# Kernel optimization log

Measured on AMD Instinct MI355X. Metric: run time of the kernel, lower is better.

Reference implementation:

```python
import jax, jax.numpy as jnp
import numpy as np

B, N, E, P, PH, H = 4, 512, 768, 64, 32, 8
D = E // H  # 96
FFN = 3072

def _ln(x, g, b, eps=1e-5):
    mu = jnp.mean(x, axis=-1, keepdims=True)
    var = jnp.mean((x - mu) ** 2, axis=-1, keepdims=True)
    return (x - mu) * jax.lax.rsqrt(var + eps) * g + b

def setup_inputs() -> dict:
    key = jax.random.key(0)
    ks = iter(jax.random.split(key, 80))
    def f(*s):
        return jax.random.normal(next(ks), s, jnp.float32) * 0.02
    ones = lambda *s: jnp.ones(s, jnp.float32)
    zeros = lambda *s: jnp.zeros(s, jnp.float32)
    return {
        'x': jax.random.normal(next(ks), (B, N, E), jnp.float32),
        'pair': jax.random.normal(next(ks), (B, N, N, P), jnp.float32) * 0.5,
        'attn_mask': zeros(B, 1, N, N),
        'op_mask': ones(B, N, 1),
        'op_norm': ones(1) / N,
        'nlist': jax.random.randint(next(ks), (B, N, 64), 0, N),
        'wq': f(E, E), 'wk': f(E, E), 'wv': f(E, E),
        'wg': f(E, E), 'bg': zeros(E),
        'wo': f(E, E), 'bo': zeros(E),
        'ln_pair_g': ones(P), 'ln_pair_b': zeros(P),
        'wb': f(H, P), 'bb': zeros(H),
        'ln_attn_g': ones(E), 'ln_attn_b': zeros(E),
        'ln_ffn_g': ones(E), 'ln_ffn_b': zeros(E),
        'w_ffn1': f(FFN, E), 'b_ffn1': zeros(FFN),
        'w_ffn2': f(E, FFN), 'b_ffn2': zeros(E),
        'ln_opm_g': ones(E), 'ln_opm_b': zeros(E),
        'w_opm_in': f(2 * PH, E), 'b_opm_in': zeros(2 * PH),
        'w_opm_out': f(P, PH * PH), 'b_opm_out': zeros(P),
        'ln_tm_g': ones(P), 'ln_tm_b': zeros(P),
        'w_tm_abp': f(2 * PH, P), 'b_tm_abp': zeros(2 * PH),
        'w_tm_abg': f(2 * PH, P), 'b_tm_abg': zeros(2 * PH),
        'w_tm_g': f(P, P), 'b_tm_g': zeros(P),
        'w_tm_z': f(P, PH), 'b_tm_z': zeros(P),
        'ln_tmo_g': ones(PH), 'ln_tmo_b': zeros(PH),
        'ln_pffn_g': ones(P), 'ln_pffn_b': zeros(P),
        'w_pffn1': f(P, P), 'b_pffn1': zeros(P),
        'w_pffn2': f(P, P), 'b_pffn2': zeros(P),
    }

def _forward(x, pair, attn_mask, op_mask, op_norm, wq, wk, wv, wg, bg, wo, bo,
             ln_pair_g, ln_pair_b, wb, bb, ln_attn_g, ln_attn_b,
             ln_ffn_g, ln_ffn_b, w_ffn1, b_ffn1, w_ffn2, b_ffn2,
             ln_opm_g, ln_opm_b, w_opm_in, b_opm_in, w_opm_out, b_opm_out,
             ln_tm_g, ln_tm_b, w_tm_abp, b_tm_abp, w_tm_abg, b_tm_abg,
             w_tm_g, b_tm_g, w_tm_z, b_tm_z, ln_tmo_g, ln_tmo_b,
             ln_pffn_g, ln_pffn_b, w_pffn1, b_pffn1, w_pffn2, b_pffn2):
    Bx, Nx, _ = x.shape
    # --- gated pair-bias self-attention (pre-LN, eval mode: dropout = identity) ---
    h = _ln(x, ln_attn_g, ln_attn_b)
    pn = _ln(pair, ln_pair_g, ln_pair_b)               # AtomAttention pair LayerNorm
    bias = jnp.einsum('bijp,hp->bhij', pn, wb) + bb[None, :, None, None]
    q = (h @ wq.T).reshape(Bx, Nx, H, D).transpose(0, 2, 1, 3) * (D ** -0.5)
    k = (h @ wk.T).reshape(Bx, Nx, H, D).transpose(0, 2, 1, 3)
    v = (h @ wv.T).reshape(Bx, Nx, H, D).transpose(0, 2, 1, 3)
    attn = jax.nn.softmax(jnp.einsum('bhid,bhjd->bhij', q, k) + attn_mask + bias, axis=-1)
    o = jnp.einsum('bhij,bhjd->bhid', attn, v).transpose(0, 2, 1, 3).reshape(Bx, Nx, E)
    o = jax.nn.sigmoid(h @ wg.T + bg) * o              # sigmoid output gate
    x = x + (o @ wo.T + bo)
    # --- atom transition MLP ---
    h = _ln(x, ln_ffn_g, ln_ffn_b)
    x = x + (jax.nn.gelu(h @ w_ffn1.T + b_ffn1, approximate=False) @ w_ffn2.T + b_ffn2)
    # --- OuterProduct pair update (fused: avoids [B,N,N,PH*PH] intermediate) ---
    h = _ln(x, ln_opm_g, ln_opm_b)
    ab = (h @ w_opm_in.T + b_opm_in) * op_mask
    a_o, b_o = jnp.split(ab, 2, axis=-1)               # each [B,N,PH]
    z = jnp.einsum('bid,bje,pde->bijp', a_o, b_o, w_opm_out.reshape(P, PH, PH)) + b_opm_out
    pair = pair + z * op_norm
    # --- triangle multiplication ---
    zp = _ln(pair, ln_tm_g, ln_tm_b)
    gpr = zp @ w_tm_g.T + b_tm_g                       # gate (no sigmoid, matches source)
    ab = (zp @ w_tm_abp.T + b_tm_abp) * jax.nn.sigmoid(zp @ w_tm_abg.T + b_tm_abg)
    a_t, b_t = jnp.split(ab, 2, axis=-1)               # each [B,N,N,PH]
    t = jnp.einsum('bijh,bkjh->bhik', a_t, b_t) + jnp.einsum('bjih,bjkh->bhik', a_t, b_t)
    t = _ln(t.transpose(0, 2, 3, 1), ln_tmo_g, ln_tmo_b) @ w_tm_z.T + b_tm_z
    pair = pair + gpr * t
    # --- pair transition MLP ---
    zp = _ln(pair, ln_pffn_g, ln_pffn_b)
    pair = pair + (jax.nn.gelu(zp @ w_pffn1.T + b_pffn1, approximate=False) @ w_pffn2.T + b_pffn2)
    return x, pair

def reference(x, pair, attn_mask, op_mask, op_norm, nlist, wq, wk, wv, wg, bg, wo, bo,
              ln_pair_g, ln_pair_b, wb, bb, ln_attn_g, ln_attn_b,
              ln_ffn_g, ln_ffn_b, w_ffn1, b_ffn1, w_ffn2, b_ffn2,
              ln_opm_g, ln_opm_b, w_opm_in, b_opm_in, w_opm_out, b_opm_out,
              ln_tm_g, ln_tm_b, w_tm_abp, b_tm_abp, w_tm_abg, b_tm_abg,
              w_tm_g, b_tm_g, w_tm_z, b_tm_z, ln_tmo_g, ln_tmo_b,
              ln_pffn_g, ln_pffn_b, w_pffn1, b_pffn1, w_pffn2, b_pffn2):
    del nlist  # accepted by the torch module but unused in the math
    return _forward(x, pair, attn_mask, op_mask, op_norm, wq, wk, wv, wg, bg, wo, bo,
                    ln_pair_g, ln_pair_b, wb, bb, ln_attn_g, ln_attn_b,
                    ln_ffn_g, ln_ffn_b, w_ffn1, b_ffn1, w_ffn2, b_ffn2,
                    ln_opm_g, ln_opm_b, w_opm_in, b_opm_in, w_opm_out, b_opm_out,
                    ln_tm_g, ln_tm_b, w_tm_abp, b_tm_abp, w_tm_abg, b_tm_abg,
                    w_tm_g, b_tm_g, w_tm_z, b_tm_z, ln_tmo_g, ln_tmo_b,
                    ln_pffn_g, ln_pffn_b, w_pffn1, b_pffn1, w_pffn2, b_pffn2)
```

## Files before the change

kernel.cpp:

```cpp
#include <hip/hip_runtime.h>
#include <hip/hip_bf16.h>
#include <math.h>

#define Nn 512
#define Ee 768
#define Pp 64
#define PHh 32
#define Hh 8
#define Dd 96
#define NNe 262144
#define LNEPS 1e-5f

typedef __attribute__((ext_vector_type(8))) short bf8;
typedef __attribute__((ext_vector_type(4))) short bf4;
typedef __attribute__((ext_vector_type(4))) float f32x4;
#define MFMA(a,b,c) __builtin_amdgcn_mfma_f32_16x16x32_bf16(a,b,c,0,0,0)

__device__ __forceinline__ short f2bf(float f) {
  unsigned u = __builtin_bit_cast(unsigned, f);
  unsigned r = (u + 0x7fffu + ((u >> 16) & 1u)) >> 16;
  return (short)r;
}
__device__ __forceinline__ float bf2f(short s) {
  unsigned u = ((unsigned)(unsigned short)s) << 16;
  return __builtin_bit_cast(float, u);
}

__device__ __forceinline__ float wave_red_sum(float v) {
#pragma unroll
  for (int off = 32; off > 0; off >>= 1) v += __shfl_xor(v, off);
  return v;
}
__device__ __forceinline__ float gelu_exact(float v) {
  return 0.5f * v * (1.f + erff(v * 0.70710678118654752f));
}
__device__ __forceinline__ float sigmoidf_(float v) {
  return 1.f / (1.f + expf(-v));
}

__global__ __launch_bounds__(256) void castw_kernel(
    const float* __restrict__ wq, const float* __restrict__ wk,
    const float* __restrict__ wv, const float* __restrict__ wg,
    const float* __restrict__ wo, const float* __restrict__ f1,
    const float* __restrict__ f2, const float* __restrict__ wop,
    short* __restrict__ dst, float qs) {
  long i = (long)blockIdx.x * 256 + threadIdx.x;
  float v;
  if (i < 589824) v = wq[i] * qs;
  else if (i < 1179648) v = wk[i - 589824];
  else if (i < 1769472) v = wv[i - 1179648];
  else if (i < 2359296) v = wg[i - 1769472];
  else if (i < 2949120) v = wo[i - 2359296];
  else if (i < 5308416) v = f1[i - 2949120];
  else if (i < 7667712) v = f2[i - 5308416];
  else if (i < 7716864) v = wop[i - 7667712];
  else return;
  dst[i] = f2bf(v);
}

__global__ __launch_bounds__(256) void castw2_kernel(
    const float* __restrict__ wb, const float* __restrict__ abp,
    const float* __restrict__ abg, const float* __restrict__ wtg,
    const float* __restrict__ wtz, const float* __restrict__ p1,
    const float* __restrict__ p2, short* __restrict__ dst) {
  int i = blockIdx.x * 256 + threadIdx.x;
  float v;
  if (i < 512) v = wb[i];
  else if (i < 4608) v = abp[i - 512];
  else if (i < 8704) v = abg[i - 4608];
  else if (i < 12800) v = wtg[i - 8704];
  else if (i < 14848) v = wtz[i - 12800];
  else if (i < 18944) v = p1[i - 14848];
  else if (i < 23040) v = p2[i - 18944];
  else return;
  dst[i] = f2bf(v);
}

__global__ __launch_bounds__(256) void ln_bf_kernel(const float* __restrict__ in,
                                                    short* __restrict__ out,
                                                    const float* __restrict__ gam,
                                                    const float* __restrict__ bet, int C) {
  int row = blockIdx.x;
  const float* xr = in + (long)row * C;
  short* yr = out + (long)row * C;
  float s = 0.f, ss = 0.f;
  for (int c = threadIdx.x; c < C; c += 256) { float v = xr[c]; s += v; ss += v * v; }
  s = wave_red_sum(s); ss = wave_red_sum(ss);
  __shared__ float sm[4][2];
  int wv = threadIdx.x >> 6, lane = threadIdx.x & 63;
  if (lane == 0) { sm[wv][0] = s; sm[wv][1] = ss; }
  __syncthreads();
  float ts = sm[0][0] + sm[1][0] + sm[2][0] + sm[3][0];
  float tss = sm[0][1] + sm[1][1] + sm[2][1] + sm[3][1];
  float mu = ts / C;
  float var = tss / C - mu * mu;
  float rs = rsqrtf(var + LNEPS);
  for (int c = threadIdx.x; c < C; c += 256) {
    float v = xr[c];
    yr[c] = f2bf((v - mu) * rs * gam[c] + bet[c]);
  }
}

__global__ __launch_bounds__(256) void gemm_bf(
    const short* __restrict__ A, int lda, long asB, long asH,
    const short* __restrict__ Bm, int ldb, long bsB, long bsH,
    float* __restrict__ outF, int ldf, long fsB, long fsH,
    short* __restrict__ outB, int ldob,
    const float* __restrict__ resid, int ldr, long rsB, long rsH,
    const float* __restrict__ bias,
    int M, int N, int K, int act, int vtrans, int Hdim) {
  int bz = blockIdx.z, bb = bz / Hdim, hh = bz % Hdim;
  A += bb * asB + hh * asH;
  Bm += bb * bsB + hh * bsH;
  if (outF) outF += bb * fsB + hh * fsH;
  if (outB) outB += bb * fsB + hh * fsH;
  if (resid) resid += bb * rsB + hh * rsH;
  __shared__ __align__(16) short As[64 * 40];
  __shared__ __align__(16) short Bs[64 * 40];
  int m0 = blockIdx.y * 64, n0 = blockIdx.x * 64;
  int tid = threadIdx.x;
  int wv = tid >> 6, lane = tid & 63;
  int wr = wv >> 1, wc = wv & 1;
  int lhi = lane >> 4, llo = lane & 15;
  int r4 = tid >> 2, c8 = (tid & 3) * 8;
  f32x4 acc[2][2] = {};
  for (int k0 = 0; k0 < K; k0 += 32) {
    *(bf8*)&As[r4 * 40 + c8] = *(const bf8*)(A + (long)(m0 + r4) * lda + k0 + c8);
    bf8 bv = {};
    if (n0 + r4 < N) bv = *(const bf8*)(Bm + (long)(n0 + r4) * ldb + k0 + c8);
    *(bf8*)&Bs[r4 * 40 + c8] = bv;
    __syncthreads();
    bf8 a0 = *(const bf8*)&As[(wr * 32 + llo) * 40 + lhi * 8];
    bf8 a1 = *(const bf8*)&As[(wr * 32 + 16 + llo) * 40 + lhi * 8];
    bf8 b0 = *(const bf8*)&Bs[(wc * 32 + llo) * 40 + lhi * 8];
    bf8 b1 = *(const bf8*)&Bs[(wc * 32 + 16 + llo) * 40 + lhi * 8];
    acc[0][0] = MFMA(a0, b0, acc[0][0]);
    acc[0][1] = MFMA(a0, b1, acc[0][1]);
    acc[1][0] = MFMA(a1, b0, acc[1][0]);
    acc[1][1] = MFMA(a1, b1, acc[1][1]);
    __syncthreads();
  }
#pragma unroll
  for (int mi = 0; mi < 2; ++mi) {
    int gmb = m0 + wr * 32 + mi * 16 + lhi * 4;
#pragma unroll
    for (int ni = 0; ni < 2; ++ni) {
      int gn = n0 + wc * 32 + ni * 16 + llo;
      if (gn >= N) continue;
      float bv = bias ? bias[gn] : 0.f;
      float vr[4];
#pragma unroll
      for (int r = 0; r < 4; ++r) {
        float v = acc[mi][ni][r] + bv;
        if (resid) {
          float rv = resid[(long)(gmb + r) * ldr + gn];
          if (act == 2) v = sigmoidf_(rv) * acc[mi][ni][r];
          else v += rv;
        }
        if (act == 1) v = gelu_exact(v);
        vr[r] = v;
      }
      if (outF) {
#pragma unroll
        for (int r = 0; r < 4; ++r) outF[(long)(gmb + r) * ldf + gn] = vr[r];
      }
      if (outB) {
        if (vtrans) {
          bf4 pk;
#pragma unroll
          for (int r = 0; r < 4; ++r) pk[r] = f2bf(vr[r]);
          *(bf4*)(outB + ((long)((gmb >> 9) * 768 + gn) * 512 + (gmb & 511))) = pk;
        } else {
#pragma unroll
          for (int r = 0; r < 4; ++r) outB[(long)(gmb + r) * ldob + gn] = f2bf(vr[r]);
        }
      }
    }
  }
}

__global__ __launch_bounds__(256) void gemm_qkvg(
    const short* __restrict__ A, const short* __restrict__ W,
    short* __restrict__ q_bf, short* __restrict__ k_bf,
    short* __restrict__ vT_bf, float* __restrict__ gb,
    const float* __restrict__ bg) {
  __shared__ __align__(16) short As[64 * 40];
  __shared__ __align__(16) short Bs[64 * 40];
  int m0 = blockIdx.y * 64, n0 = blockIdx.x * 64;
  int sec = n0 / 768;
  int cbase = n0 - sec * 768;
  int tid = threadIdx.x;
  int wv = tid >> 6, lane = tid & 63;
  int wr = wv >> 1, wc = wv & 1;
  int lhi = lane >> 4, llo = lane & 15;
  int r4 = tid >> 2, c8 = (tid & 3) * 8;
  f32x4 acc[2][2] = {};
  for (int k0 = 0; k0 < 768; k0 += 32) {
    *(bf8*)&As[r4 * 40 + c8] = *(const bf8*)(A + (long)(m0 + r4) * 768 + k0 + c8);
    *(bf8*)&Bs[r4 * 40 + c8] = *(const bf8*)(W + (long)(n0 + r4) * 768 + k0 + c8);
    __syncthreads();
    bf8 a0 = *(const bf8*)&As[(wr * 32 + llo) * 40 + lhi * 8];
    bf8 a1 = *(const bf8*)&As[(wr * 32 + 16 + llo) * 40 + lhi * 8];
    bf8 b0 = *(const bf8*)&Bs[(wc * 32 + llo) * 40 + lhi * 8];
    bf8 b1 = *(const bf8*)&Bs[(wc * 32 + 16 + llo) * 40 + lhi * 8];
    acc[0][0] = MFMA(a0, b0, acc[0][0]);
    acc[0][1] = MFMA(a0, b1, acc[0][1]);
    acc[1][0] = MFMA(a1, b0, acc[1][0]);
    acc[1][1] = MFMA(a1, b1, acc[1][1]);
    __syncthreads();
  }
#pragma unroll
  for (int mi = 0; mi < 2; ++mi) {
    int gmb = m0 + wr * 32 + mi * 16 + lhi * 4;
#pragma unroll
    for (int ni = 0; ni < 2; ++ni) {
      int cn = cbase + wc * 32 + ni * 16 + llo;
      if (sec == 0) {
#pragma unroll
        for (int r = 0; r < 4; ++r) q_bf[(long)(gmb + r) * 768 + cn] = f2bf(acc[mi][ni][r]);
      } else if (sec == 1) {
#pragma unroll
        for (int r = 0; r < 4; ++r) k_bf[(long)(gmb + r) * 768 + cn] = f2bf(acc[mi][ni][r]);
      } else if (sec == 2) {
        bf4 pk;
#pragma unroll
        for (int r = 0; r < 4; ++r) pk[r] = f2bf(acc[mi][ni][r]);
        *(bf4*)(vT_bf + ((long)((gmb >> 9) * 768 + cn) * 512 + (gmb & 511))) = pk;
      } else {
        float bv = bg[cn];
#pragma unroll
        for (int r = 0; r < 4; ++r) gb[(long)(gmb + r) * 768 + cn] = acc[mi][ni][r] + bv;
      }
    }
  }
}

__global__ __launch_bounds__(256) void attn_fused(
    const short* __restrict__ q_bf, const short* __restrict__ k_bf,
    const short* __restrict__ bias_bf, const float* __restrict__ mask,
    short* __restrict__ out_bf) {
  int it = blockIdx.x, h = blockIdx.y, b = blockIdx.z;
  int tid = threadIdx.x;
  int wv = tid >> 6, lane = tid & 63;
  int lhi = lane >> 4, llo = lane & 15;
  int i0 = it * 16;
  long qoff = ((long)(b * 512 + i0)) * 768 + h * 96;
  bf8 qf[3];
#pragma unroll
  for (int ks = 0; ks < 3; ++ks)
    qf[ks] = *(const bf8*)(q_bf + qoff + (long)llo * 768 + ks * 32 + lhi * 8);
  long koff = ((long)b * 512) * 768 + h * 96;
  long bioff = (long)(b * 8 + h) * NNe + (long)i0 * 512;
  long moff = (long)b * NNe + (long)i0 * 512;
  float sv[8][4];
  int jb0 = wv * 128;
#pragma unroll
  for (int jf = 0; jf < 8; ++jf) {
    int jb = jb0 + jf * 16;
    f32x4 acc = {0.f, 0.f, 0.f, 0.f};
#pragma unroll
    for (int ks = 0; ks < 3; ++ks) {
      bf8 kf = *(const bf8*)(k_bf + koff + (long)(jb + llo) * 768 + ks * 32 + lhi * 8);
      acc = MFMA(qf[ks], kf, acc);
    }
#pragma unroll
    for (int r = 0; r < 4; ++r) {
      int irow = lhi * 4 + r;
      int j = jb + llo;
      float bia = bf2f(bias_bf[bioff + (long)irow * 512 + j]);
      float mk = mask[moff + (long)irow * 512 + j];
      sv[jf][r] = acc[r] + bia + mk;
    }
  }
  __shared__ float redA[4][20];
  __shared__ float redB[4][20];
  float rmax[4];
#pragma unroll
  for (int r = 0; r < 4; ++r) {
    float m = sv[0][r];
#pragma unroll
    for (int jf = 1; jf < 8; ++jf) m = fmaxf(m, sv[jf][r]);
#pragma unroll
    for (int off = 1; off < 16; off <<= 1) m = fmaxf(m, __shfl_xor(m, off, 16));
    if (llo == 0) redA[wv][lhi * 4 + r] = m;
  }
  __syncthreads();
#pragma unroll
  for (int r = 0; r < 4; ++r) {
    int row = lhi * 4 + r;
    rmax[r] = fmaxf(fmaxf(redA[0][row], redA[1][row]),
                    fmaxf(redA[2][row], redA[3][row]));
  }
  float rsum[4] = {0.f, 0.f, 0.f, 0.f};
#pragma unroll
  for (int jf = 0; jf < 8; ++jf)
#pragma unroll
    for (int r = 0; r < 4; ++r) {
      float e = __expf(sv[jf][r] - rmax[r]);
      sv[jf][r] = e;
      rsum[r] += e;
    }
#pragma unroll
  for (int r = 0; r < 4; ++r) {
#pragma unroll
    for (int off = 1; off < 16; off <<= 1) rsum[r] += __shfl_xor(rsum[r], off, 16);
    if (llo == 0) redB[wv][lhi * 4 + r] = rsum[r];
  }
  __syncthreads();
#pragma unroll
  for (int r = 0; r < 4; ++r) {
    int row = lhi * 4 + r;
    float s = redB[0][row] + redB[1][row] + redB[2][row] + redB[3][row];
    float inv = 1.f / s;
#pragma unroll
    for (int jf = 0; jf < 8; ++jf) {
      int j = jb0 + jf * 16 + llo;
      out_bf[bioff + (long)row * 512 + j] = f2bf(sv[jf][r] * inv);
    }
  }
}

__global__ __launch_bounds__(256) void opmask_kernel(float* __restrict__ ab,
                                                     const float* __restrict__ mask,
                                                     short* __restrict__ bo_bf) {
  int idx = blockIdx.x * 256 + threadIdx.x;
  if (idx < 131072) {
    float v = ab[idx] * mask[idx >> 6];
    ab[idx] = v;
    int ch = idx & 63;
    if (ch >= 32) bo_bf[(idx >> 6) * 32 + ch - 32] = f2bf(v);
  }
}

__global__ __launch_bounds__(256) void opm_T_kernel(const float* __restrict__ ab,
                                                    const float* __restrict__ w,
                                                    short* __restrict__ T) {
  int p = blockIdx.y;
  int row = blockIdx.x * 8 + threadIdx.y;
  int e = threadIdx.x;
  const float* a = ab + (long)row * 64;
  const float* wp = w + p * 1024 + e;
  float acc = 0.f;
#pragma unroll
  for (int d = 0; d < 32; ++d) acc += a[d] * wp[d * 32];
  T[((long)row * 64 + p) * 32 + e] = f2bf(acc);
}

__global__ __launch_bounds__(256) void pair_bias_mfma(
    const float* __restrict__ pair, const float* __restrict__ gam,
    const float* __restrict__ bet, const short* __restrict__ wb_a,
    const float* __restrict__ bbv, short* __restrict__ bias) {
  __shared__ __align__(16) short Zb[64 * 72];
  __shared__ __align__(16) short Wb[16 * 72];
  __shared__ float sp[4][2][72];
  int tid = threadIdx.x;
  long e0 = (long)blockIdx.x * 64;
  int b = (int)(e0 >> 18);
  long ein = e0 & (NNe - 1);
  const float* base = pair + e0 * 64;
  for (int l = tid; l < 1024; l += 256) {
    int h = l >> 6, c = l & 63;
    Wb[h * 72 + c] = (h < 8) ? wb_a[h * 64 + c] : (short)0;
  }
  int e = tid & 63, q = tid >> 6;
  f32x4 v4[4];
  float s = 0.f, ss = 0.f;
#pragma unroll
  for (int k = 0; k < 4; ++k) {
    v4[k] = *(const f32x4*)(base + (long)e * 64 + q * 16 + k * 4);
#pragma unroll
    for (int u = 0; u < 4; ++u) { float v = v4[k][u]; s += v; ss += v * v; }
  }
  sp[q][0][e] = s; sp[q][1][e] = ss;
  __syncthreads();
  float ts = sp[0][0][e] + sp[1][0][e] + sp[2][0][e] + sp[3][0][e];
  float tss = sp[0][1][e] + sp[1][1][e] + sp[2][1][e] + sp[3][1][e];
  float mu = ts * 0.015625f, var = tss * 0.015625f - mu * mu;
  float rs = rsqrtf(var + LNEPS);
#pragma unroll
  for (int k = 0; k < 4; ++k) {
    bf4 pk;
#pragma unroll
    for (int u = 0; u < 4; ++u) {
      int c = q * 16 + k * 4 + u;
      pk[u] = f2bf((v4[k][u] - mu) * rs * gam[c] + bet[c]);
    }
    *(bf4*)&Zb[e * 72 + q * 16 + k * 4] = pk;
  }
  __syncthreads();
  int wv = tid >> 6, lane = tid & 63;
  int lhi = lane >> 4, llo = lane & 15;
  int n0 = wv * 16;
  f32x4 acc = {0.f, 0.f, 0.f, 0.f};
#pragma unroll
  for (int ks = 0; ks < 2; ++ks) {
    bf8 a = *(const bf8*)&Wb[llo * 72 + ks * 32 + lhi * 8];
    bf8 bz = *(const bf8*)&Zb[(n0 + llo) * 72 + ks * 32 + lhi * 8];
    acc = MFMA(a, bz, acc);
  }
  int elem = n0 + llo;
#pragma unroll
  for (int r = 0; r < 4; ++r) {
    int h = lhi * 4 + r;
    if (h < 8) bias[(long)(b * 8 + h) * NNe + ein + elem] = f2bf(acc[r] + bbv[h]);
  }
}

__global__ __launch_bounds__(256) void opm_ab_fused(
    const float* __restrict__ pair_in, const short* __restrict__ Tb,
    const short* __restrict__ bo_bf, const float* __restrict__ b_out,
    const float* __restrict__ op_norm, const float* __restrict__ gam,
    const float* __restrict__ bet, const short* __restrict__ wp_a,
    const float* __restrict__ b_abp, const short* __restrict__ wg_a,
    const float* __restrict__ b_abg, float* __restrict__ pair1,
    short* __restrict__ aN, short* __restrict__ bN) {
  int jt = blockIdx.x;
  int i = blockIdx.y;
  int tid = threadIdx.x;
  __shared__ __align__(16) short Tsb[64 * 40];
  __shared__ __align__(16) short Bob[64 * 40];
  __shared__ __align__(16) short Zb[64 * 72];
  __shared__ __align__(16) short Wp[64 * 72];
  __shared__ __align__(16) short Wg[64 * 72];
  __shared__ float spS[64][9];
  __shared__ float spQ[64][9];
  int wv = tid >> 6, lane = tid & 63;
  int wr = wv >> 1, wc = wv & 1;
  int lhi = lane >> 4, llo = lane & 15;
  int chb = wr * 32 + lhi * 4;
  {
    int p = tid >> 2, e8 = (tid & 3) * 8;
    *(bf8*)&Tsb[p * 40 + e8] = *(const bf8*)(Tb + (long)i * 2048 + p * 32 + e8);
    *(bf8*)&Bob[p * 40 + e8] = *(const bf8*)(bo_bf + (long)(jt * 64 + p) * 32 + e8);
  }
  for (int l = tid; l < 512; l += 256) {
    int r = l >> 3, c8 = (l & 7) * 8;
    *(bf8*)&Wp[r * 72 + c8] = *(const bf8*)(wp_a + r * 64 + c8);
    *(bf8*)&Wg[r * 72 + c8] = *(const bf8*)(wg_a + r * 64 + c8);
  }
  long ebase = (long)i * 512 + jt * 64;
  const float* pbase = pair_in + ebase * 64;
  f32x4 x[2][2];
#pragma unroll
  for (int mi = 0; mi < 2; ++mi)
#pragma unroll
    for (int ni = 0; ni < 2; ++ni)
      x[mi][ni] = *(const f32x4*)(pbase + (long)(wc * 32 + ni * 16 + llo) * 64 +
                                  chb + mi * 16);
  __syncthreads();
  f32x4 acc[2][2] = {};
  {
    bf8 a0 = *(const bf8*)&Tsb[(wr * 32 + llo) * 40 + lhi * 8];
    bf8 a1 = *(const bf8*)&Tsb[(wr * 32 + 16 + llo) * 40 + lhi * 8];
    bf8 b0 = *(const bf8*)&Bob[(wc * 32 + llo) * 40 + lhi * 8];
    bf8 b1 = *(const bf8*)&Bob[(wc * 32 + 16 + llo) * 40 + lhi * 8];
    acc[0][0] = MFMA(a0, b0, acc[0][0]);
    acc[0][1] = MFMA(a0, b1, acc[0][1]);
    acc[1][0] = MFMA(a1, b0, acc[1][0]);
    acc[1][1] = MFMA(a1, b1, acc[1][1]);
  }
  float nrm = op_norm[0];
#pragma unroll
  for (int mi = 0; mi < 2; ++mi) {
    f32x4 bo4 = *(const f32x4*)(b_out + chb + mi * 16);
#pragma unroll
    for (int ni = 0; ni < 2; ++ni)
#pragma unroll
      for (int r = 0; r < 4; ++r)
        x[mi][ni][r] += (acc[mi][ni][r] + bo4[r]) * nrm;
  }
#pragma unroll
  for (int mi = 0; mi < 2; ++mi)
#pragma unroll
    for (int ni = 0; ni < 2; ++ni)
      *(f32x4*)(pair1 + (ebase + wc * 32 + ni * 16 + llo) * 64 + chb + mi * 16) =
          x[mi][ni];
#pragma unroll
  for (int ni = 0; ni < 2; ++ni) {
    float s = 0.f, ss = 0.f;
#pragma unroll
    for (int mi = 0; mi < 2; ++mi)
#pragma unroll
      for (int r = 0; r < 4; ++r) { float v = x[mi][ni][r]; s += v; ss += v * v; }
    int e = wc * 32 + ni * 16 + llo;
    spS[e][wr * 4 + lhi] = s;
    spQ[e][wr * 4 + lhi] = ss;
  }
  __syncthreads();
  float mu1[2], rs1[2];
#pragma unroll
  for (int ni = 0; ni < 2; ++ni) {
    int e = wc * 32 + ni * 16 + llo;
    float s = 0.f, q2 = 0.f;
#pragma unroll
    for (int k = 0; k < 8; ++k) { s += spS[e][k]; q2 += spQ[e][k]; }
    float mu = s * 0.015625f, var = q2 * 0.015625f - mu * mu;
    mu1[ni] = mu; rs1[ni] = rsqrtf(var + LNEPS);
  }
#pragma unroll
  for (int mi = 0; mi < 2; ++mi) {
    f32x4 gv = *(const f32x4*)(gam + chb + mi * 16);
    f32x4 bv = *(const f32x4*)(bet + chb + mi * 16);
#pragma unroll
    for (int ni = 0; ni < 2; ++ni) {
      int e = wc * 32 + ni * 16 + llo;
      bf4 pk;
#pragma unroll
      for (int r = 0; r < 4; ++r)
        pk[r] = f2bf((x[mi][ni][r] - mu1[ni]) * rs1[ni] * gv[r] + bv[r]);
      *(bf4*)&Zb[e * 72 + chb + mi * 16] = pk;
    }
  }
  __syncthreads();
  f32x4 ap[2][2] = {};
  f32x4 ag[2][2] = {};
#pragma unroll
  for (int ks = 0; ks < 2; ++ks) {
    bf8 z0 = *(const bf8*)&Zb[(wr * 32 + llo) * 72 + ks * 32 + lhi * 8];
    bf8 z1 = *(const bf8*)&Zb[(wr * 32 + 16 + llo) * 72 + ks * 32 + lhi * 8];
    bf8 p0 = *(const bf8*)&Wp[(wc * 32 + llo) * 72 + ks * 32 + lhi * 8];
    bf8 p1 = *(const bf8*)&Wp[(wc * 32 + 16 + llo) * 72 + ks * 32 + lhi * 8];
    bf8 g0 = *(const bf8*)&Wg[(wc * 32 + llo) * 72 + ks * 32 + lhi * 8];
    bf8 g1 = *(const bf8*)&Wg[(wc * 32 + 16 + llo) * 72 + ks * 32 + lhi * 8];
    ap[0][0] = MFMA(z0, p0, ap[0][0]);
    ap[0][1] = MFMA(z0, p1, ap[0][1]);
    ap[1][0] = MFMA(z1, p0, ap[1][0]);
    ap[1][1] = MFMA(z1, p1, ap[1][1]);
    ag[0][0] = MFMA(z0, g0, ag[0][0]);
    ag[0][1] = MFMA(z0, g1, ag[0][1]);
    ag[1][0] = MFMA(z1, g0, ag[1][0]);
    ag[1][1] = MFMA(z1, g1, ag[1][1]);
  }
#pragma unroll
  for (int mi = 0; mi < 2; ++mi) {
    int elemb = wr * 32 + mi * 16 + lhi * 4;
#pragma unroll
    for (int ni = 0; ni < 2; ++ni) {
      int ch = wc * 32 + ni * 16 + llo;
      float bp = b_abp[ch], bg = b_abg[ch];
      bf4 pack;
#pragma unroll
      for (int r = 0; r < 4; ++r)
        pack[r] = f2bf((ap[mi][ni][r] + bp) * sigmoidf_(ag[mi][ni][r] + bg));
      short* dst = (ch < 32) ? (aN + (long)ch * NNe) : (bN + (long)(ch - 32) * NNe);
      *(bf4*)(dst + ebase + elemb) = pack;
    }
  }
}

__global__ __launch_bounds__(256) void tm_tri_mfma(const short* __restrict__ aN,
                                                   const short* __restrict__ bN,
                                                   short* __restrict__ t_out) {
  int h = blockIdx.z;
  int i0 = blockIdx.y * 64, k0 = blockIdx.x * 64;
  const short* A = aN + (long)h * NNe;
  const short* B = bN + (long)h * NNe;
  __shared__ __align__(16) short A1[64 * 40];
  __shared__ __align__(16) short B1[64 * 40];
  __shared__ __align__(16) short A2[64 * 40];
  __shared__ __align__(16) short B2[64 * 40];
  int tid = threadIdx.x;
  int wv = tid >> 6, lane = tid & 63;
  int wr = wv >> 1, wc = wv & 1;
  int lhi = lane >> 4, llo = lane & 15;
  int r1 = tid >> 2, cp = (tid & 3) * 8;
  int s2 = tid >> 4;
  int cg = (tid & 15) * 4;
  f32x4 acc[2][2] = {};
  for (int j0 = 0; j0 < 512; j0 += 32) {
    *(bf8*)&A1[r1 * 40 + cp] = *(const bf8*)(A + (long)(i0 + r1) * 512 + j0 + cp);
    *(bf8*)&B1[r1 * 40 + cp] = *(const bf8*)(B + (long)(k0 + r1) * 512 + j0 + cp);
    bf4 va0 = *(const bf4*)(A + (long)(j0 + 2 * s2) * 512 + i0 + cg);
    bf4 va1 = *(const bf4*)(A + (long)(j0 + 2 * s2 + 1) * 512 + i0 + cg);
    bf4 vb0 = *(const bf4*)(B + (long)(j0 + 2 * s2) * 512 + k0 + cg);
    bf4 vb1 = *(const bf4*)(B + (long)(j0 + 2 * s2 + 1) * 512 + k0 + cg);
#pragma unroll
    for (int q = 0; q < 4; ++q) {
      unsigned pa = (unsigned)(unsigned short)va0[q] |
                    ((unsigned)(unsigned short)va1[q] << 16);
      unsigned pb = (unsigned)(unsigned short)vb0[q] |
                    ((unsigned)(unsigned short)vb1[q] << 16);
      *(unsigned*)&A2[(cg + q) * 40 + 2 * s2] = pa;
      *(unsigned*)&B2[(cg + q) * 40 + 2 * s2] = pb;
    }
    __syncthreads();
    bf8 a0 = *(const bf8*)&A1[(wr * 32 + llo) * 40 + lhi * 8];
    bf8 a1 = *(const bf8*)&A1[(wr * 32 + 16 + llo) * 40 + lhi * 8];
    bf8 b0 = *(const bf8*)&B1[(wc * 32 + llo) * 40 + lhi * 8];
    bf8 b1 = *(const bf8*)&B1[(wc * 32 + 16 + llo) * 40 + lhi * 8];
    acc[0][0] = MFMA(a0, b0, acc[0][0]);
    acc[0][1] = MFMA(a0, b1, acc[0][1]);
    acc[1][0] = MFMA(a1, b0, acc[1][0]);
    acc[1][1] = MFMA(a1, b1, acc[1][1]);
    bf8 c0 = *(const bf8*)&A2[(wr * 32 + llo) * 40 + lhi * 8];
    bf8 c1 = *(const bf8*)&A2[(wr * 32 + 16 + llo) * 40 + lhi * 8];
    bf8 d0 = *(const bf8*)&B2[(wc * 32 + llo) * 40 + lhi * 8];
    bf8 d1 = *(const bf8*)&B2[(wc * 32 + 16 + llo) * 40 + lhi * 8];
    acc[0][0] = MFMA(c0, d0, acc[0][0]);
    acc[0][1] = MFMA(c0, d1, acc[0][1]);
    acc[1][0] = MFMA(c1, d0, acc[1][0]);
    acc[1][1] = MFMA(c1, d1, acc[1][1]);
    __syncthreads();
  }
  short* tp = t_out + (long)h * NNe;
#pragma unroll
  for (int mi = 0; mi < 2; ++mi)
#pragma unroll
    for (int ni = 0; ni < 2; ++ni) {
      int row = i0 + wr * 32 + mi * 16 + lhi * 4;
      int col = k0 + wc * 32 + ni * 16 + llo;
#pragma unroll
      for (int r = 0; r < 4; ++r) tp[(long)(row + r) * 512 + col] = f2bf(acc[mi][ni][r]);
    }
}

__global__ __launch_bounds__(256) void upd_pffn_fused(
    float* __restrict__ pb, const short* __restrict__ t_in,
    const float* __restrict__ g_tm, const float* __restrict__ b_tm,
    const short* __restrict__ wg_a, const float* __restrict__ b_g,
    const short* __restrict__ wz_a, const float* __restrict__ b_z,
    const float* __restrict__ g_tmo, const float* __restrict__ b_tmo,
    const float* __restrict__ g_pf, const float* __restrict__ b_pf,
    const short* __restrict__ w1_a, const float* __restrict__ b1,
    const short* __restrict__ w2_a, const float* __restrict__ b2) {
  __shared__ __align__(16) short Zb[64 * 72];
  __shared__ __align__(16) short Tlb[64 * 40];
  __shared__ __align__(16) short Wbuf[64 * 72];
  __shared__ __align__(16) short Wzb[64 * 40];
  __shared__ float spS[64][9];
  __shared__ float spQ[64][9];
  __shared__ float spB[4][2][72];
  int tid = threadIdx.x;
  long e0 = (long)blockIdx.x * 64;
  float* base = pb + e0 * 64;
  int wv = tid >> 6, lane = tid & 63;
  int wr = wv >> 1, wc = wv & 1;
  int lhi = lane >> 4, llo = lane & 15;
  int chb = wr * 32 + lhi * 4;
  int r0 = tid >> 3, c0 = (tid & 7) * 8;
  int r1 = (tid + 256) >> 3, c1 = ((tid + 256) & 7) * 8;
  bf8 w1r0, w1r1, w2r0, w2r1;
  {
    *(bf8*)&Wbuf[r0 * 72 + c0] = *(const bf8*)(wg_a + r0 * 64 + c0);
    *(bf8*)&Wbuf[r1 * 72 + c1] = *(const bf8*)(wg_a + r1 * 64 + c1);
    w1r0 = *(const bf8*)(w1_a + r0 * 64 + c0);
    w1r1 = *(const bf8*)(w1_a + r1 * 64 + c1);
    w2r0 = *(const bf8*)(w2_a + r0 * 64 + c0);
    w2r1 = *(const bf8*)(w2_a + r1 * 64 + c1);
    int rz = tid >> 2, cz = (tid & 3) * 8;
    *(bf8*)&Wzb[rz * 40 + cz] = *(const bf8*)(wz_a + rz * 32 + cz);
  }
  f32x4 x[2][2];
#pragma unroll
  for (int mi = 0; mi < 2; ++mi)
#pragma unroll
    for (int ni = 0; ni < 2; ++ni)
      x[mi][ni] = *(const f32x4*)(base + (long)(wc * 32 + ni * 16 + llo) * 64 +
                                  chb + mi * 16);
#pragma unroll
  for (int ni = 0; ni < 2; ++ni) {
    float s = 0.f, ss = 0.f;
#pragma unroll
    for (int mi = 0; mi < 2; ++mi)
#pragma unroll
      for (int r = 0; r < 4; ++r) { float v = x[mi][ni][r]; s += v; ss += v * v; }
    int e = wc * 32 + ni * 16 + llo;
    spS[e][wr * 4 + lhi] = s;
    spQ[e][wr * 4 + lhi] = ss;
  }
  int te = tid & 63, tq = tid >> 6;
  float tt[8];
  {
    float sB = 0.f, ssB = 0.f;
#pragma unroll
    for (int k = 0; k < 8; ++k) {
      float v = bf2f(t_in[(long)(tq * 8 + k) * NNe + e0 + te]);
      tt[k] = v; sB += v; ssB += v * v;
    }
    spB[tq][0][te] = sB; spB[tq][1][te] = ssB;
  }
  __syncthreads();
  {
    float ts = spB[0][0][te] + spB[1][0][te] + spB[2][0][te] + spB[3][0][te];
    float tss = spB[0][1][te] + spB[1][1][te] + spB[2][1][te] + spB[3][1][te];
    float mu = ts * 0.03125f, var = tss * 0.03125f - mu * mu;
    float rs = rsqrtf(var + LNEPS);
    bf8 pk;
#pragma unroll
    for (int k = 0; k < 8; ++k) {
      int c = tq * 8 + k;
      pk[k] = f2bf((tt[k] - mu) * rs * g_tmo[c] + b_tmo[c]);
    }
    *(bf8*)&Tlb[te * 40 + tq * 8] = pk;
  }
  float mu1[2], rs1[2];
#pragma unroll
  for (int ni = 0; ni < 2; ++ni) {
    int e = wc * 32 + ni * 16 + llo;
    float s = 0.f, q2 = 0.f;
#pragma unroll
    for (int k = 0; k < 8; ++k) { s += spS[e][k]; q2 += spQ[e][k]; }
    float mu = s * 0.015625f, var = q2 * 0.015625f - mu * mu;
    mu1[ni] = mu; rs1[ni] = rsqrtf(var + LNEPS);
  }
#pragma unroll
  for (int mi = 0; mi < 2; ++mi) {
    f32x4 gv = *(const f32x4*)(g_tm + chb + mi * 16);
    f32x4 bv = *(const f32x4*)(b_tm + chb + mi * 16);
#pragma unroll
    for (int ni = 0; ni < 2; ++ni) {
      int e = wc * 32 + ni * 16 + llo;
      bf4 pk;
#pragma unroll
      for (int r = 0; r < 4; ++r)
        pk[r] = f2bf((x[mi][ni][r] - mu1[ni]) * rs1[ni] * gv[r] + bv[r]);
      *(bf4*)&Zb[e * 72 + chb + mi * 16] = pk;
    }
  }
  __syncthreads();
  f32x4 accg[2][2] = {};
  f32x4 accz[2][2] = {};
#pragma unroll
  for (int ks = 0; ks < 2; ++ks) {
    bf8 a0 = *(const bf8*)&Wbuf[(wr * 32 + llo) * 72 + ks * 32 + lhi * 8];
    bf8 a1 = *(const bf8*)&Wbuf[(wr * 32 + 16 + llo) * 72 + ks * 32 + lhi * 8];
    bf8 z0 = *(const bf8*)&Zb[(wc * 32 + llo) * 72 + ks * 32 + lhi * 8];
    bf8 z1 = *(const bf8*)&Zb[(wc * 32 + 16 + llo) * 72 + ks * 32 + lhi * 8];
    accg[0][0] = MFMA(a0, z0, accg[0][0]);
    accg[0][1] = MFMA(a0, z1, accg[0][1]);
    accg[1][0] = MFMA(a1, z0, accg[1][0]);
    accg[1][1] = MFMA(a1, z1, accg[1][1]);
  }
  {
    bf8 a0 = *(const bf8*)&Wzb[(wr * 32 + llo) * 40 + lhi * 8];
    bf8 a1 = *(const bf8*)&Wzb[(wr * 32 + 16 + llo) * 40 + lhi * 8];
    bf8 t0 = *(const bf8*)&Tlb[(wc * 32 + llo) * 40 + lhi * 8];
    bf8 t1 = *(const bf8*)&Tlb[(wc * 32 + 16 + llo) * 40 + lhi * 8];
    accz[0][0] = MFMA(a0, t0, accz[0][0]);
    accz[0][1] = MFMA(a0, t1, accz[0][1]);
    accz[1][0] = MFMA(a1, t0, accz[1][0]);
    accz[1][1] = MFMA(a1, t1, accz[1][1]);
  }
#pragma unroll
  for (int mi = 0; mi < 2; ++mi) {
    f32x4 bgv = *(const f32x4*)(b_g + chb + mi * 16);
    f32x4 bzv = *(const f32x4*)(b_z + chb + mi * 16);
#pragma unroll
    for (int ni = 0; ni < 2; ++ni)
#pragma unroll
      for (int r = 0; r < 4; ++r)
        x[mi][ni][r] += (accg[mi][ni][r] + bgv[r]) * (accz[mi][ni][r] + bzv[r]);
  }
#pragma unroll
  for (int ni = 0; ni < 2; ++ni) {
    float s = 0.f, ss = 0.f;
#pragma unroll
    for (int mi = 0; mi < 2; ++mi)
#pragma unroll
      for (int r = 0; r < 4; ++r) { float v = x[mi][ni][r]; s += v; ss += v * v; }
    int e = wc * 32 + ni * 16 + llo;
    spS[e][wr * 4 + lhi] = s;
    spQ[e][wr * 4 + lhi] = ss;
  }
  __syncthreads();
  *(bf8*)&Wbuf[r0 * 72 + c0] = w1r0;
  *(bf8*)&Wbuf[r1 * 72 + c1] = w1r1;
#pragma unroll
  for (int ni = 0; ni < 2; ++ni) {
    int e = wc * 32 + ni * 16 + llo;
    float s = 0.f, q2 = 0.f;
#pragma unroll
    for (int k = 0; k < 8; ++k) { s += spS[e][k]; q2 += spQ[e][k]; }
    float mu = s * 0.015625f, var = q2 * 0.015625f - mu * mu;
    mu1[ni] = mu; rs1[ni] = rsqrtf(var + LNEPS);
  }
#pragma unroll
  for (int mi = 0; mi < 2; ++mi) {
    f32x4 gv = *(const f32x4*)(g_pf + chb + mi * 16);
    f32x4 bv = *(const f32x4*)(b_pf + chb + mi * 16);
#pragma unroll
    for (int ni = 0; ni < 2; ++ni) {
      int e = wc * 32 + ni * 16 + llo;
      bf4 pk;
#pragma unroll
      for (int r = 0; r < 4; ++r)
        pk[r] = f2bf((x[mi][ni][r] - mu1[ni]) * rs1[ni] * gv[r] + bv[r]);
      *(bf4*)&Zb[e * 72 + chb + mi * 16] = pk;
    }
  }
  __syncthreads();
  f32x4 acc1[2][2] = {};
#pragma unroll
  for (int ks = 0; ks < 2; ++ks) {
    bf8 a0 = *(const bf8*)&Wbuf[(wr * 32 + llo) * 72 + ks * 32 + lhi * 8];
    bf8 a1 = *(const bf8*)&Wbuf[(wr * 32 + 16 + llo) * 72 + ks * 32 + lhi * 8];
    bf8 z0 = *(const bf8*)&Zb[(wc * 32 + llo) * 72 + ks * 32 + lhi * 8];
    bf8 z1 = *(const bf8*)&Zb[(wc * 32 + 16 + llo) * 72 + ks * 32 + lhi * 8];
    acc1[0][0] = MFMA(a0, z0, acc1[0][0]);
    acc1[0][1] = MFMA(a0, z1, acc1[0][1]);
    acc1[1][0] = MFMA(a1, z0, acc1[1][0]);
    acc1[1][1] = MFMA(a1, z1, acc1[1][1]);
  }
  __syncthreads();
  *(bf8*)&Wbuf[r0 * 72 + c0] = w2r0;
  *(bf8*)&Wbuf[r1 * 72 + c1] = w2r1;
#pragma unroll
  for (int mi = 0; mi < 2; ++mi) {
    f32x4 bv = *(const f32x4*)(b1 + chb + mi * 16);
#pragma unroll
    for (int ni = 0; ni < 2; ++ni) {
      int e = wc * 32 + ni * 16 + llo;
      bf4 pk;
#pragma unroll
      for (int r = 0; r < 4; ++r) pk[r] = f2bf(gelu_exact(acc1[mi][ni][r] + bv[r]));
      *(bf4*)&Zb[e * 72 + chb + mi * 16] = pk;
    }
  }
  __syncthreads();
  f32x4 acc2[2][2] = {};
#pragma unroll
  for (int ks = 0; ks < 2; ++ks) {
    bf8 a0 = *(const bf8*)&Wbuf[(wr * 32 + llo) * 72 + ks * 32 + lhi * 8];
    bf8 a1 = *(const bf8*)&Wbuf[(wr * 32 + 16 + llo) * 72 + ks * 32 + lhi * 8];
    bf8 z0 = *(const bf8*)&Zb[(wc * 32 + llo) * 72 + ks * 32 + lhi * 8];
    bf8 z1 = *(const bf8*)&Zb[(wc * 32 + 16 + llo) * 72 + ks * 32 + lhi * 8];
    acc2[0][0] = MFMA(a0, z0, acc2[0][0]);
    acc2[0][1] = MFMA(a0, z1, acc2[0][1]);
    acc2[1][0] = MFMA(a1, z0, acc2[1][0]);
    acc2[1][1] = MFMA(a1, z1, acc2[1][1]);
  }
#pragma unroll
  for (int mi = 0; mi < 2; ++mi) {
    f32x4 bv = *(const f32x4*)(b2 + chb + mi * 16);
#pragma unroll
    for (int ni = 0; ni < 2; ++ni) {
#pragma unroll
      for (int r = 0; r < 4; ++r) x[mi][ni][r] += acc2[mi][ni][r] + bv[r];
      *(f32x4*)(base + (long)(wc * 32 + ni * 16 + llo) * 64 + chb + mi * 16) =
          x[mi][ni];
    }
  }
}

extern "C" void kernel_launch(void* const* d_in, const int* in_sizes, int n_in,
                              void* d_out, int out_size, void* d_ws, size_t ws_size,
                              hipStream_t stream) {
  const float* x = (const float*)d_in[0];
  const float* pair = (const float*)d_in[1];
  const float* attn_mask = (const float*)d_in[2];
  const float* op_mask = (const float*)d_in[3];
  const float* op_norm = (const float*)d_in[4];
  const float* wq = (const float*)d_in[6];
  const float* wk = (const float*)d_in[7];
  const float* wv_ = (const float*)d_in[8];
  const float* wg = (const float*)d_in[9];
  const float* bg = (const float*)d_in[10];
  const float* wo = (const float*)d_in[11];
  const float* bo = (const float*)d_in[12];
  const float* ln_pair_g = (const float*)d_in[13];
  const float* ln_pair_b = (const float*)d_in[14];
  const float* wb = (const float*)d_in[15];
  const float* bb = (const float*)d_in[16];
  const float* ln_attn_g = (const float*)d_in[17];
  const float* ln_attn_b = (const float*)d_in[18];
  const float* ln_ffn_g = (const float*)d_in[19];
  const float* ln_ffn_b = (const float*)d_in[20];
  const float* w_ffn1 = (const float*)d_in[21];
  const float* b_ffn1 = (const float*)d_in[22];
  const float* w_ffn2 = (const float*)d_in[23];
  const float* b_ffn2 = (const float*)d_in[24];
  const float* ln_opm_g = (const float*)d_in[25];
  const float* ln_opm_b = (const float*)d_in[26];
  const float* w_opm_in = (const float*)d_in[27];
  const float* b_opm_in = (const float*)d_in[28];
  const float* w_opm_out = (const float*)d_in[29];
  const float* b_opm_out = (const float*)d_in[30];
  const float* ln_tm_g = (const float*)d_in[31];
  const float* ln_tm_b = (const float*)d_in[32];
  const float* w_tm_abp = (const float*)d_in[33];
  const float* b_tm_abp = (const float*)d_in[34];
  const float* w_tm_abg = (const float*)d_in[35];
  const float* b_tm_abg = (const float*)d_in[36];
  const float* w_tm_g = (const float*)d_in[37];
  const float* b_tm_g = (const float*)d_in[38];
  const float* w_tm_z = (const float*)d_in[39];
  const float* b_tm_z = (const float*)d_in[40];
  const float* ln_tmo_g = (const float*)d_in[41];
  const float* ln_tmo_b = (const float*)d_in[42];
  const float* ln_pffn_g = (const float*)d_in[43];
  const float* ln_pffn_b = (const float*)d_in[44];
  const float* w_pffn1 = (const float*)d_in[45];
  const float* b_pffn1 = (const float*)d_in[46];
  const float* w_pffn2 = (const float*)d_in[47];
  const float* b_pffn2 = (const float*)d_in[48];

  float* ws = (float*)d_ws;
  short* wbf = (short*)ws;
  short* wq_bf = wbf + 0;
  short* wo_bf = wbf + 2359296;
  short* wf1_bf = wbf + 2949120;
  short* wf2_bf = wbf + 5308416;
  short* wop_bf = wbf + 7667712;
  short* wb_a = wbf + 7716864;
  short* wabp_a = wbf + 7717376;
  short* wabg_a = wbf + 7721472;
  short* wtg_a = wbf + 7725568;
  short* wtz_a = wbf + 7729664;
  short* wp1_a = wbf + 7731712;
  short* wp2_a = wbf + 7735808;

  short* h_bf = (short*)(ws + 3869952);
  short* q_bf = (short*)(ws + 4656384);
  short* k_bf = (short*)(ws + 5442816);
  short* vT_bf = (short*)(ws + 6229248);
  float* gb = ws + 7015680;
  short* gb_bf = (short*)(ws + 10161408);
  float* x1b = ws + 10947840;
  short* biasb_bf = (short*)(ws + 12520704);
  short* attn_bf = (short*)(ws + 16715008);
  short* mffn_bf = (short*)(ws + 20909312);
  float* abb = ws + 24055040;
  short* abb_bf = (short*)(ws + 24186112);
  short* Tb_bf = (short*)(ws + 24218880);
  short* aNb = (short*)(ws + 4656384);
  short* bNb = (short*)(ws + 8850688);
  short* t_bf = (short*)(ws + 13044992);

  float* xo = (float*)d_out;
  float* pair1 = xo + 1572864;

  const float qscale = 0.1020620726159658f;

  castw_kernel<<<30144, 256, 0, stream>>>(wq, wk, wv_, wg, wo, w_ffn1, w_ffn2, w_opm_in,
                                          wbf, qscale);
  castw2_kernel<<<90, 256, 0, stream>>>(wb, w_tm_abp, w_tm_abg, w_tm_g, w_tm_z,
                                        w_pffn1, w_pffn2, wb_a);
  ln_bf_kernel<<<2048, 256, 0, stream>>>(x, h_bf, ln_attn_g, ln_attn_b, 768);
  gemm_qkvg<<<dim3(48, 32, 1), 256, 0, stream>>>(h_bf, wq_bf, q_bf, k_bf, vT_bf, gb, bg);
  pair_bias_mfma<<<16384, 256, 0, stream>>>(pair, ln_pair_g, ln_pair_b, wb_a, bb, biasb_bf);
  attn_fused<<<dim3(32, 8, 4), 256, 0, stream>>>(q_bf, k_bf, biasb_bf, attn_mask, attn_bf);
  gemm_bf<<<dim3(2, 8, 32), 256, 0, stream>>>(attn_bf, 512, 2097152, 262144,
                                              vT_bf, 512, 393216, 49152,
                                              nullptr, 0, 393216, 96, gb_bf, 768,
                                              gb, 768, 393216, 96, nullptr,
                                              512, 96, 512, 2, 0, 8);
  gemm_bf<<<dim3(12, 32, 1), 256, 0, stream>>>(gb_bf, 768, 0, 0, wo_bf, 768, 0, 0,
                                               x1b, 768, 0, 0, nullptr, 0,
                                               x, 768, 0, 0, bo,
                                               2048, 768, 768, 0, 0, 1);
  ln_bf_kernel<<<2048, 256, 0, stream>>>(x1b, h_bf, ln_ffn_g, ln_ffn_b, 768);
  gemm_bf<<<dim3(48, 32, 1), 256, 0, stream>>>(h_bf, 768, 0, 0, wf1_bf, 768, 0, 0,
                                               nullptr, 0, 0, 0, mffn_bf, 3072,
                                               nullptr, 0, 0, 0, b_ffn1,
                                               2048, 3072, 768, 1, 0, 1);
  gemm_bf<<<dim3(12, 32, 1), 256, 0, stream>>>(mffn_bf, 3072, 0, 0, wf2_bf, 3072, 0, 0,
                                               xo, 768, 0, 0, nullptr, 0,
                                               x1b, 768, 0, 0, b_ffn2,
                                               2048, 768, 3072, 0, 0, 1);
  ln_bf_kernel<<<2048, 256, 0, stream>>>(xo, h_bf, ln_opm_g, ln_opm_b, 768);
  gemm_bf<<<dim3(1, 32, 1), 256, 0, stream>>>(h_bf, 768, 0, 0, wop_bf, 768, 0, 0,
                                              abb, 64, 0, 0, nullptr, 0,
                                              nullptr, 0, 0, 0, b_opm_in,
                                              2048, 64, 768, 0, 0, 1);
  opmask_kernel<<<512, 256, 0, stream>>>(abb, op_mask, abb_bf);
  opm_T_kernel<<<dim3(256, 64, 1), dim3(32, 8, 1), 0, stream>>>(abb, w_opm_out, Tb_bf);
  for (int b = 0; b < 4; ++b) {
    const float* pin = pair + (long)b * NNe * 64;
    float* pbb = pair1 + (long)b * NNe * 64;
    opm_ab_fused<<<dim3(8, 512, 1), 256, 0, stream>>>(
        pin, Tb_bf + (long)b * 1048576, abb_bf + (long)b * 16384, b_opm_out, op_norm,
        ln_tm_g, ln_tm_b, wabp_a, b_tm_abp, wabg_a, b_tm_abg, pbb, aNb, bNb);
    tm_tri_mfma<<<dim3(8, 8, 32), 256, 0, stream>>>(aNb, bNb, t_bf);
    upd_pffn_fused<<<4096, 256, 0, stream>>>(
        pbb, t_bf, ln_tm_g, ln_tm_b, wtg_a, b_tm_g, wtz_a, b_tm_z,
        ln_tmo_g, ln_tmo_b, ln_pffn_g, ln_pffn_b, wp1_a, b_pffn1, wp2_a, b_pffn2);
  }
}
```

Measured before the change: 987.2 us.

## Double K-step in GEMMs and enlarge triangle-multiply tiles to 128x128

The generic and QKVG GEMMs now stage 64-wide K slices per iteration and issue two MFMA k-steps per barrier pair, which halves the number of synchronisations. The triangle-multiply kernel moves from 64x64 to 128x128 output tiles with 512 threads, so each wave computes a 64x32 block and reuses its B fragments across four A fragments. This cuts global and LDS traffic per output. The cost is more LDS and registers per block and a much smaller grid for tm_tri (512 blocks instead of 2048), which may reduce latency hiding.

```diff
diff --git a/kernel.cpp b/kernel.cpp
--- a/kernel.cpp
+++ b/kernel.cpp
@@ -115,8 +115,8 @@
   if (outF) outF += bb * fsB + hh * fsH;
   if (outB) outB += bb * fsB + hh * fsH;
   if (resid) resid += bb * rsB + hh * rsH;
-  __shared__ __align__(16) short As[64 * 40];
-  __shared__ __align__(16) short Bs[64 * 40];
+  __shared__ __align__(16) short As[64 * 72];
+  __shared__ __align__(16) short Bs[64 * 72];
   int m0 = blockIdx.y * 64, n0 = blockIdx.x * 64;
   int tid = threadIdx.x;
   int wv = tid >> 6, lane = tid & 63;
@@ -124,20 +124,29 @@
   int lhi = lane >> 4, llo = lane & 15;
   int r4 = tid >> 2, c8 = (tid & 3) * 8;
   f32x4 acc[2][2] = {};
-  for (int k0 = 0; k0 < K; k0 += 32) {
-    *(bf8*)&As[r4 * 40 + c8] = *(const bf8*)(A + (long)(m0 + r4) * lda + k0 + c8);
-    bf8 bv = {};
-    if (n0 + r4 < N) bv = *(const bf8*)(Bm + (long)(n0 + r4) * ldb + k0 + c8);
-    *(bf8*)&Bs[r4 * 40 + c8] = bv;
+  for (int k0 = 0; k0 < K; k0 += 64) {
+    *(bf8*)&As[r4 * 72 + c8] = *(const bf8*)(A + (long)(m0 + r4) * lda + k0 + c8);
+    *(bf8*)&As[r4 * 72 + 32 + c8] =
+        *(const bf8*)(A + (long)(m0 + r4) * lda + k0 + 32 + c8);
+    bf8 bv0 = {}, bv1 = {};
+    if (n0 + r4 < N) {
+      bv0 = *(const bf8*)(Bm + (long)(n0 + r4) * ldb + k0 + c8);
+      bv1 = *(const bf8*)(Bm + (long)(n0 + r4) * ldb + k0 + 32 + c8);
+    }
+    *(bf8*)&Bs[r4 * 72 + c8] = bv0;
+    *(bf8*)&Bs[r4 * 72 + 32 + c8] = bv1;
     __syncthreads();
-    bf8 a0 = *(const bf8*)&As[(wr * 32 + llo) * 40 + lhi * 8];
-    bf8 a1 = *(const bf8*)&As[(wr * 32 + 16 + llo) * 40 + lhi * 8];
-    bf8 b0 = *(const bf8*)&Bs[(wc * 32 + llo) * 40 + lhi * 8];
-    bf8 b1 = *(const bf8*)&Bs[(wc * 32 + 16 + llo) * 40 + lhi * 8];
-    acc[0][0] = MFMA(a0, b0, acc[0][0]);
-    acc[0][1] = MFMA(a0, b1, acc[0][1]);
-    acc[1][0] = MFMA(a1, b0, acc[1][0]);
-    acc[1][1] = MFMA(a1, b1, acc[1][1]);
+#pragma unroll
+    for (int ks = 0; ks < 2; ++ks) {
+      bf8 a0 = *(const bf8*)&As[(wr * 32 + llo) * 72 + ks * 32 + lhi * 8];
+      bf8 a1 = *(const bf8*)&As[(wr * 32 + 16 + llo) * 72 + ks * 32 + lhi * 8];
+      bf8 b0 = *(const bf8*)&Bs[(wc * 32 + llo) * 72 + ks * 32 + lhi * 8];
+      bf8 b1 = *(const bf8*)&Bs[(wc * 32 + 16 + llo) * 72 + ks * 32 + lhi * 8];
+      acc[0][0] = MFMA(a0, b0, acc[0][0]);
+      acc[0][1] = MFMA(a0, b1, acc[0][1]);
+      acc[1][0] = MFMA(a1, b0, acc[1][0]);
+      acc[1][1] = MFMA(a1, b1, acc[1][1]);
+    }
     __syncthreads();
   }
 #pragma unroll
@@ -184,8 +193,8 @@
     short* __restrict__ q_bf, short* __restrict__ k_bf,
     short* __restrict__ vT_bf, float* __restrict__ gb,
     const float* __restrict__ bg) {
-  __shared__ __align__(16) short As[64 * 40];
-  __shared__ __align__(16) short Bs[64 * 40];
+  __shared__ __align__(16) short As[64 * 72];
+  __shared__ __align__(16) short Bs[64 * 72];
   int m0 = blockIdx.y * 64, n0 = blockIdx.x * 64;
   int sec = n0 / 768;
   int cbase = n0 - sec * 768;
@@ -195,18 +204,25 @@
   int lhi = lane >> 4, llo = lane & 15;
   int r4 = tid >> 2, c8 = (tid & 3) * 8;
   f32x4 acc[2][2] = {};
-  for (int k0 = 0; k0 < 768; k0 += 32) {
-    *(bf8*)&As[r4 * 40 + c8] = *(const bf8*)(A + (long)(m0 + r4) * 768 + k0 + c8);
-    *(bf8*)&Bs[r4 * 40 + c8] = *(const bf8*)(W + (long)(n0 + r4) * 768 + k0 + c8);
+  for (int k0 = 0; k0 < 768; k0 += 64) {
+    *(bf8*)&As[r4 * 72 + c8] = *(const bf8*)(A + (long)(m0 + r4) * 768 + k0 + c8);
+    *(bf8*)&As[r4 * 72 + 32 + c8] =
+        *(const bf8*)(A + (long)(m0 + r4) * 768 + k0 + 32 + c8);
+    *(bf8*)&Bs[r4 * 72 + c8] = *(const bf8*)(W + (long)(n0 + r4) * 768 + k0 + c8);
+    *(bf8*)&Bs[r4 * 72 + 32 + c8] =
+        *(const bf8*)(W + (long)(n0 + r4) * 768 + k0 + 32 + c8);
     __syncthreads();
-    bf8 a0 = *(const bf8*)&As[(wr * 32 + llo) * 40 + lhi * 8];
-    bf8 a1 = *(const bf8*)&As[(wr * 32 + 16 + llo) * 40 + lhi * 8];
-    bf8 b0 = *(const bf8*)&Bs[(wc * 32 + llo) * 40 + lhi * 8];
-    bf8 b1 = *(const bf8*)&Bs[(wc * 32 + 16 + llo) * 40 + lhi * 8];
-    acc[0][0] = MFMA(a0, b0, acc[0][0]);
-    acc[0][1] = MFMA(a0, b1, acc[0][1]);
-    acc[1][0] = MFMA(a1, b0, acc[1][0]);
-    acc[1][1] = MFMA(a1, b1, acc[1][1]);
+#pragma unroll
+    for (int ks = 0; ks < 2; ++ks) {
+      bf8 a0 = *(const bf8*)&As[(wr * 32 + llo) * 72 + ks * 32 + lhi * 8];
+      bf8 a1 = *(const bf8*)&As[(wr * 32 + 16 + llo) * 72 + ks * 32 + lhi * 8];
+      bf8 b0 = *(const bf8*)&Bs[(wc * 32 + llo) * 72 + ks * 32 + lhi * 8];
+      bf8 b1 = *(const bf8*)&Bs[(wc * 32 + 16 + llo) * 72 + ks * 32 + lhi * 8];
+      acc[0][0] = MFMA(a0, b0, acc[0][0]);
+      acc[0][1] = MFMA(a0, b1, acc[0][1]);
+      acc[1][0] = MFMA(a1, b0, acc[1][0]);
+      acc[1][1] = MFMA(a1, b1, acc[1][1]);
+    }
     __syncthreads();
   }
 #pragma unroll
@@ -548,25 +564,24 @@
   }
 }
 
-__global__ __launch_bounds__(256) void tm_tri_mfma(const short* __restrict__ aN,
+__global__ __launch_bounds__(512) void tm_tri_mfma(const short* __restrict__ aN,
                                                    const short* __restrict__ bN,
                                                    short* __restrict__ t_out) {
   int h = blockIdx.z;
-  int i0 = blockIdx.y * 64, k0 = blockIdx.x * 64;
+  int i0 = blockIdx.y * 128, k0 = blockIdx.x * 128;
   const short* A = aN + (long)h * NNe;
   const short* B = bN + (long)h * NNe;
-  __shared__ __align__(16) short A1[64 * 40];
-  __shared__ __align__(16) short B1[64 * 40];
-  __shared__ __align__(16) short A2[64 * 40];
-  __shared__ __align__(16) short B2[64 * 40];
+  __shared__ __align__(16) short A1[128 * 40];
+  __shared__ __align__(16) short B1[128 * 40];
+  __shared__ __align__(16) short A2[128 * 40];
+  __shared__ __align__(16) short B2[128 * 40];
   int tid = threadIdx.x;
   int wv = tid >> 6, lane = tid & 63;
-  int wr = wv >> 1, wc = wv & 1;
+  int wr = wv >> 2, wc = wv & 3;
   int lhi = lane >> 4, llo = lane & 15;
   int r1 = tid >> 2, cp = (tid & 3) * 8;
-  int s2 = tid >> 4;
-  int cg = (tid & 15) * 4;
-  f32x4 acc[2][2] = {};
+  int s2 = tid >> 5, cg = (tid & 31) * 4;
+  f32x4 acc[4][2] = {};
   for (int j0 = 0; j0 < 512; j0 += 32) {
     *(bf8*)&A1[r1 * 40 + cp] = *(const bf8*)(A + (long)(i0 + r1) * 512 + j0 + cp);
     *(bf8*)&B1[r1 * 40 + cp] = *(const bf8*)(B + (long)(k0 + r1) * 512 + j0 + cp);
@@ -584,30 +599,32 @@
       *(unsigned*)&B2[(cg + q) * 40 + 2 * s2] = pb;
     }
     __syncthreads();
-    bf8 a0 = *(const bf8*)&A1[(wr * 32 + llo) * 40 + lhi * 8];
-    bf8 a1 = *(const bf8*)&A1[(wr * 32 + 16 + llo) * 40 + lhi * 8];
-    bf8 b0 = *(const bf8*)&B1[(wc * 32 + llo) * 40 + lhi * 8];
-    bf8 b1 = *(const bf8*)&B1[(wc * 32 + 16 + llo) * 40 + lhi * 8];
-    acc[0][0] = MFMA(a0, b0, acc[0][0]);
-    acc[0][1] = MFMA(a0, b1, acc[0][1]);
-    acc[1][0] = MFMA(a1, b0, acc[1][0]);
-    acc[1][1] = MFMA(a1, b1, acc[1][1]);
-    bf8 c0 = *(const bf8*)&A2[(wr * 32 + llo) * 40 + lhi * 8];
-    bf8 c1 = *(const bf8*)&A2[(wr * 32 + 16 + llo) * 40 + lhi * 8];
-    bf8 d0 = *(const bf8*)&B2[(wc * 32 + llo) * 40 + lhi * 8];
-    bf8 d1 = *(const bf8*)&B2[(wc * 32 + 16 + llo) * 40 + lhi * 8];
-    acc[0][0] = MFMA(c0, d0, acc[0][0]);
-    acc[0][1] = MFMA(c0, d1, acc[0][1]);
-    acc[1][0] = MFMA(c1, d0, acc[1][0]);
-    acc[1][1] = MFMA(c1, d1, acc[1][1]);
+    bf8 bfr[2], dfr[2];
+#pragma unroll
+    for (int ni = 0; ni < 2; ++ni) {
+      bfr[ni] = *(const bf8*)&B1[(wc * 32 + ni * 16 + llo) * 40 + lhi * 8];
+      dfr[ni] = *(const bf8*)&B2[(wc * 32 + ni * 16 + llo) * 40 + lhi * 8];
+    }
+#pragma unroll
+    for (int mi = 0; mi < 4; ++mi) {
+      bf8 a = *(const bf8*)&A1[(wr * 64 + mi * 16 + llo) * 40 + lhi * 8];
+      acc[mi][0] = MFMA(a, bfr[0], acc[mi][0]);
+      acc[mi][1] = MFMA(a, bfr[1], acc[mi][1]);
+    }
+#pragma unroll
+    for (int mi = 0; mi < 4; ++mi) {
+      bf8 c = *(const bf8*)&A2[(wr * 64 + mi * 16 + llo) * 40 + lhi * 8];
+      acc[mi][0] = MFMA(c, dfr[0], acc[mi][0]);
+      acc[mi][1] = MFMA(c, dfr[1], acc[mi][1]);
+    }
     __syncthreads();
   }
   short* tp = t_out + (long)h * NNe;
 #pragma unroll
-  for (int mi = 0; mi < 2; ++mi)
+  for (int mi = 0; mi < 4; ++mi)
 #pragma unroll
     for (int ni = 0; ni < 2; ++ni) {
-      int row = i0 + wr * 32 + mi * 16 + lhi * 4;
+      int row = i0 + wr * 64 + mi * 16 + lhi * 4;
       int col = k0 + wc * 32 + ni * 16 + llo;
 #pragma unroll
       for (int r = 0; r < 4; ++r) tp[(long)(row + r) * 512 + col] = f2bf(acc[mi][ni][r]);
@@ -970,7 +987,7 @@
     opm_ab_fused<<<dim3(8, 512, 1), 256, 0, stream>>>(
         pin, Tb_bf + (long)b * 1048576, abb_bf + (long)b * 16384, b_opm_out, op_norm,
         ln_tm_g, ln_tm_b, wabp_a, b_tm_abp, wabg_a, b_tm_abg, pbb, aNb, bNb);
-    tm_tri_mfma<<<dim3(8, 8, 32), 256, 0, stream>>>(aNb, bNb, t_bf);
+    tm_tri_mfma<<<dim3(4, 4, 32), 512, 0, stream>>>(aNb, bNb, t_bf);
     upd_pffn_fused<<<4096, 256, 0, stream>>>(
         pbb, t_bf, ln_tm_g, ln_tm_b, wtg_a, b_tm_g, wtz_a, b_tm_z,
         ln_tmo_g, ln_tmo_b, ln_pffn_g, ln_pffn_b, wp1_a, b_pffn1, wp2_a, b_pffn2);
```

Measured after the change: 949.8 us. 1.04x faster.
